# Kernel optimization log

Measured on AMD Instinct MI355X. Metric: run time of the kernel, lower is better.

The kernel has to match this reference:

```python
import jax, jax.numpy as jnp
import numpy as np


def _relative_position_index(w):
    # Deterministic Swin relative-position index, shape [w*w, w*w], values in [0, (2w-1)^2)
    coords_h = np.arange(w)
    coords_w = np.arange(w)
    coords = np.stack(np.meshgrid(coords_h, coords_w, indexing="ij"))  # [2, w, w]
    coords = coords.reshape(2, -1)                                      # [2, w*w]
    rel = coords[:, :, None] - coords[:, None, :]                       # [2, N, N]
    rel = rel.transpose(1, 2, 0).copy()                                 # [N, N, 2]
    rel[:, :, 0] += w - 1
    rel[:, :, 1] += w - 1
    rel[:, :, 0] *= 2 * w - 1
    return jnp.asarray(rel.sum(-1), dtype=jnp.int32)


def setup_inputs() -> dict:
    key = jax.random.key(0)
    ks = jax.random.split(key, 7)
    BS, N, C, H, W = 4096, 49, 384, 12, 7
    NW = 64  # number of windows per image
    x = jax.random.normal(ks[0], (BS, N, C), dtype=jnp.float32)
    # Swin shift mask: 0 where attention allowed, -100 where blocked
    u = jax.random.uniform(ks[1], (NW, N, N))
    mask = jnp.where(u < 0.5, 0.0, -100.0).astype(jnp.float32)
    qkv_w = jax.random.normal(ks[2], (C, 3 * C), dtype=jnp.float32) * (C ** -0.5)
    qkv_b = jax.random.normal(ks[3], (3 * C,), dtype=jnp.float32) * 0.02
    proj_w = jax.random.normal(ks[4], (C, C), dtype=jnp.float32) * (C ** -0.5)
    proj_b = jax.random.normal(ks[5], (C,), dtype=jnp.float32) * 0.02
    bias_table = jax.random.normal(ks[6], ((2 * W - 1) ** 2, H), dtype=jnp.float32) * 0.02
    return {"x": x, "mask": mask, "qkv_w": qkv_w, "qkv_b": qkv_b,
            "proj_w": proj_w, "proj_b": proj_b, "bias_table": bias_table,
            "n_heads": 12, "window_size": 7}


def reference(x, mask, qkv_w, qkv_b, proj_w, proj_b, bias_table, n_heads, window_size):
    BS, N, C = x.shape
    Hh = n_heads
    hd = C // Hh
    scale = hd ** -0.5
    rpi = _relative_position_index(window_size)  # [N, N] int

    qkv = x @ qkv_w + qkv_b                       # [BS, N, 3C]
    qkv = qkv.reshape(BS, N, 3, Hh, hd).transpose(2, 0, 3, 1, 4)  # [3, BS, H, N, hd]
    q, k, v = qkv[0], qkv[1], qkv[2]

    attn = jnp.einsum("bhnd,bhmd->bhnm", q, k) * scale   # [BS, H, N, N]
    # relative position bias gather: [N*N, H] -> [H, N, N]
    rpb = bias_table[rpi.reshape(-1)].reshape(N, N, Hh).transpose(2, 0, 1)
    attn = attn + rpb[None]

    nw = mask.shape[0]
    attn = attn.reshape(BS // nw, nw, Hh, N, N) + mask[None, :, None]
    attn = attn.reshape(BS, Hh, N, N)

    attn = jax.nn.softmax(attn, axis=-1)
    out = jnp.einsum("bhnm,bhmd->bhnd", attn, v)          # [BS, H, N, hd]
    out = out.transpose(0, 2, 1, 3).reshape(BS, N, C)
    return out @ proj_w + proj_b
```

## Files before the change

### kernel.cpp

```cpp
#include <hip/hip_runtime.h>
#include <hip/hip_bf16.h>


typedef __attribute__((ext_vector_type(8))) short bf16x8;
typedef __attribute__((ext_vector_type(4))) float f32x4;

#define SEQ_N  49
#define CH     384
#define QKV_N  1152
#define HDIM   32
#define UNIT_ROWS 3136

__device__ __forceinline__ unsigned short f2b(float f) {
    union { float f; unsigned int u; } v; v.f = f;
    return (unsigned short)((v.u + 0x7FFFu + ((v.u >> 16) & 1u)) >> 16);
}

__device__ __forceinline__ bf16x8 ld8(const unsigned short* p) {
    return *(const bf16x8*)p;
}

__device__ __forceinline__ void gload16(const unsigned short* g, unsigned short* l) {
    __builtin_amdgcn_global_load_lds(
        (const __attribute__((address_space(1))) unsigned int*)g,
        (__attribute__((address_space(3))) unsigned int*)l, 16, 0, 0);
}

__device__ __forceinline__ int xcd_swizzle(int orig, int T) {
    int q = T >> 3, r = T & 7;
    int xcd = orig & 7, idx = orig >> 3;
    return (xcd < r ? xcd * (q + 1) : r * (q + 1) + (xcd - r) * q) + idx;
}

__global__ __launch_bounds__(256) void k_cvt_w(const float* __restrict__ wq,
        const float* __restrict__ wp, unsigned short* __restrict__ oq,
        unsigned short* __restrict__ op)
{
    int t = blockIdx.x * 256 + threadIdx.x;
    if (t < QKV_N * CH) {
        int n = t / CH, k = t - n * CH;
        oq[t] = f2b(wq[(size_t)k * QKV_N + n]);
    }
    if (t < CH * CH) {
        int n = t / CH, k = t - n * CH;
        op[t] = f2b(wp[(size_t)k * CH + n]);
    }
}

__global__ __launch_bounds__(256) void k_cvt(const float* __restrict__ in,
        unsigned short* __restrict__ outp, int n8)
{
    int stride = gridDim.x * 256;
    for (int i = blockIdx.x * 256 + threadIdx.x; i < n8; i += stride) {
        const float4* p = (const float4*)(in + (size_t)i * 8);
        float4 a = p[0], b = p[1];
        uint4 v;
        v.x = (unsigned)f2b(a.x) | ((unsigned)f2b(a.y) << 16);
        v.y = (unsigned)f2b(a.z) | ((unsigned)f2b(a.w) << 16);
        v.z = (unsigned)f2b(b.x) | ((unsigned)f2b(b.y) << 16);
        v.w = (unsigned)f2b(b.z) | ((unsigned)f2b(b.w) << 16);
        *(uint4*)(outp + (size_t)i * 8) = v;
    }
}

template<int OUTF32>
__global__ __launch_bounds__(256) void k_gemm(
        const unsigned short* __restrict__ A, int lda,
        const unsigned short* __restrict__ Bt, int K,
        const float* __restrict__ bias,
        unsigned short* __restrict__ Cb, float* __restrict__ Cf, int ldc,
        int M, int ntiles, int mtiles)
{
    __shared__ unsigned short As[3 * 4096];
    __shared__ unsigned short Bs[3 * 4096];
    const int wg = xcd_swizzle(blockIdx.x, mtiles * ntiles);
    const int m0 = (wg / ntiles) * 128;
    const int n0 = (wg % ntiles) * 128;
    const int tid = threadIdx.x;
    const int lane = tid & 63, wid = tid >> 6;
    const int wm = (wid >> 1) * 64, wn = (wid & 1) * 64;
    const int l15 = lane & 15, g = lane >> 4;

    f32x4 acc[4][4];
#pragma unroll
    for (int a = 0; a < 4; ++a)
#pragma unroll
        for (int b = 0; b < 4; ++b) acc[a][b] = (f32x4){0.f, 0.f, 0.f, 0.f};

    const int r0 = wid * 16 + (lane >> 2);
    const int kofs = (lane & 3) * 8;
    int ra0 = m0 + r0;       if (ra0 > M - 1) ra0 = M - 1;
    int ra1 = m0 + 64 + r0;  if (ra1 > M - 1) ra1 = M - 1;
    const unsigned short* a0p = A + (size_t)ra0 * lda + kofs;
    const unsigned short* a1p = A + (size_t)ra1 * lda + kofs;
    const unsigned short* b0p = Bt + (size_t)(n0 + r0) * K + kofs;
    const unsigned short* b1p = Bt + (size_t)(n0 + 64 + r0) * K + kofs;
    const int lo = wid * 512;

#define STAGE(kt, buf) do {                                   \
        gload16(a0p + (kt), &As[(buf) * 4096 + lo]);          \
        gload16(a1p + (kt), &As[(buf) * 4096 + 2048 + lo]);   \
        gload16(b0p + (kt), &Bs[(buf) * 4096 + lo]);          \
        gload16(b1p + (kt), &Bs[(buf) * 4096 + 2048 + lo]);   \
    } while (0)

#define COMPUTE(buf) do {                                                     \
        bf16x8 af[4], bfr[4];                                                 \
        _Pragma("unroll")                                                     \
        for (int mt = 0; mt < 4; ++mt)                                        \
            af[mt] = ld8(&As[(buf) * 4096 + (wm + mt * 16 + l15) * 32 + g * 8]); \
        _Pragma("unroll")                                                     \
        for (int nt = 0; nt < 4; ++nt)                                        \
            bfr[nt] = ld8(&Bs[(buf) * 4096 + (wn + nt * 16 + l15) * 32 + g * 8]); \
        _Pragma("unroll")                                                     \
        for (int mt = 0; mt < 4; ++mt)                                        \
            _Pragma("unroll")                                                 \
            for (int nt = 0; nt < 4; ++nt)                                    \
                acc[mt][nt] = __builtin_amdgcn_mfma_f32_16x16x32_bf16(        \
                        af[mt], bfr[nt], acc[mt][nt], 0, 0, 0);               \
    } while (0)

    const int nsteps = K >> 5;

    STAGE(0, 0);
    STAGE(32, 1);

    int cur = 0;
    for (int t = 0; t < nsteps - 2; ++t) {
        int pf = cur + 2; if (pf >= 3) pf -= 3;
        STAGE((t + 2) * 32, pf);
        __builtin_amdgcn_sched_barrier(0);
        asm volatile("s_waitcnt vmcnt(8)" ::: "memory");
        __builtin_amdgcn_sched_barrier(0);
        __builtin_amdgcn_s_barrier();
        __builtin_amdgcn_sched_barrier(0);
        COMPUTE(cur);
        __builtin_amdgcn_sched_barrier(0);
        __builtin_amdgcn_s_barrier();
        __builtin_amdgcn_sched_barrier(0);
        cur = (cur == 2) ? 0 : cur + 1;
    }
    asm volatile("s_waitcnt vmcnt(4)" ::: "memory");
    __builtin_amdgcn_sched_barrier(0);
    __builtin_amdgcn_s_barrier();
    __builtin_amdgcn_sched_barrier(0);
    COMPUTE(cur);
    cur = (cur == 2) ? 0 : cur + 1;
    asm volatile("s_waitcnt vmcnt(0)" ::: "memory");
    __builtin_amdgcn_sched_barrier(0);
    __builtin_amdgcn_s_barrier();
    __builtin_amdgcn_sched_barrier(0);
    COMPUTE(cur);
#undef STAGE
#undef COMPUTE

#pragma unroll
    for (int mt = 0; mt < 4; ++mt)
#pragma unroll
        for (int nt = 0; nt < 4; ++nt) {
            int col = n0 + wn + nt * 16 + l15;
            float bb = bias[col];
#pragma unroll
            for (int r = 0; r < 4; ++r) {
                int row = m0 + wm + mt * 16 + g * 4 + r;
                if (row < M) {
                    if (OUTF32)
                        Cf[(size_t)row * ldc + col] = acc[mt][nt][r] + bb;
                    else
                        Cb[(size_t)row * ldc + col] = f2b(acc[mt][nt][r] + bb);
                }
            }
        }
}

__global__ __launch_bounds__(256) void k_attn(unsigned short* __restrict__ qkv,
        const float* __restrict__ mask, const float* __restrict__ btab, int win_base)
{
    extern __shared__ unsigned short sm[];
    const int tid = threadIdx.x;
    const int lane = tid & 63, wv = tid >> 6;
    const int l15 = lane & 15, g = lane >> 4;
    const int pair = blockIdx.x * 4 + wv;
    const int winloc = pair / 12;
    const int h = pair - winloc * 12;
    const int wimg = (win_base + winloc) & 63;
    const int co = h * HDIM;
    unsigned short* Vt = sm + wv * 6912;
    unsigned short* Pw = Vt + 32 * 72;
    unsigned short* src = qkv + (size_t)winloc * SEQ_N * QKV_N;

    for (int t = lane; t < 32 * 16; t += 64) {
        int c = t >> 4, kk = 48 + (t & 15);
        Vt[c * 72 + kk] = 0;
    }
    for (int t = lane; t < 49 * 4; t += 64) {
        int row = t >> 2, cb = (t & 3) * 8;
        const unsigned short* vp = src + (size_t)row * QKV_N + 768 + co + cb;
        ushort4 a = ((const ushort4*)vp)[0];
        ushort4 b = ((const ushort4*)vp)[1];
        Vt[(cb + 0) * 72 + row] = a.x; Vt[(cb + 1) * 72 + row] = a.y;
        Vt[(cb + 2) * 72 + row] = a.z; Vt[(cb + 3) * 72 + row] = a.w;
        Vt[(cb + 4) * 72 + row] = b.x; Vt[(cb + 5) * 72 + row] = b.y;
        Vt[(cb + 6) * 72 + row] = b.z; Vt[(cb + 7) * 72 + row] = b.w;
    }

    bf16x8 qf[4], kf[4];
#pragma unroll
    for (int mt = 0; mt < 4; ++mt) {
        int r = mt * 16 + l15; if (r > 48) r = 48;
        qf[mt] = ld8(src + (size_t)r * QKV_N + co + g * 8);
    }
#pragma unroll
    for (int nt = 0; nt < 4; ++nt) {
        int r = nt * 16 + l15; if (r > 48) r = 48;
        kf[nt] = ld8(src + (size_t)r * QKV_N + CH + co + g * 8);
    }

    f32x4 sa[4][4];
#pragma unroll
    for (int mt = 0; mt < 4; ++mt)
#pragma unroll
        for (int nt = 0; nt < 4; ++nt) sa[mt][nt] = (f32x4){0.f, 0.f, 0.f, 0.f};
#pragma unroll
    for (int mt = 0; mt < 4; ++mt)
#pragma unroll
        for (int nt = 0; nt < 4; ++nt)
            sa[mt][nt] = __builtin_amdgcn_mfma_f32_16x16x32_bf16(
                    qf[mt], kf[nt], sa[mt][nt], 0, 0, 0);

    int jj[4], jh[4], jw4[4];
#pragma unroll
    for (int nt = 0; nt < 4; ++nt) {
        int j = nt * 16 + l15;
        jj[nt] = j; jh[nt] = j / 7; jw4[nt] = j - (j / 7) * 7;
    }
    const float scale = 0.17677669529663687f;
#pragma unroll
    for (int mt = 0; mt < 4; ++mt) {
#pragma unroll
        for (int r = 0; r < 4; ++r) {
            int i = mt * 16 + g * 4 + r;
            int ic = i < 49 ? i : 48;
            int ih = ic / 7, iw = ic - (ic / 7) * 7;
            const float* mrow = mask + (size_t)wimg * 2401 + ic * 49;
            float sv[4];
#pragma unroll
            for (int nt = 0; nt < 4; ++nt) {
                float s = sa[mt][nt][r];
                if (jj[nt] < 49) {
                    int idx = (ih - jh[nt] + 6) * 13 + (iw - jw4[nt] + 6);
                    s = s * scale + btab[idx * 12 + h] + mrow[jj[nt]];
                } else s = -1e30f;
                sv[nt] = s;
            }
            float mx = fmaxf(fmaxf(sv[0], sv[1]), fmaxf(sv[2], sv[3]));
#pragma unroll
            for (int d = 1; d < 16; d <<= 1) mx = fmaxf(mx, __shfl_xor(mx, d));
            float sum = 0.f;
#pragma unroll
            for (int nt = 0; nt < 4; ++nt) { sv[nt] = __expf(sv[nt] - mx); sum += sv[nt]; }
#pragma unroll
            for (int d = 1; d < 16; d <<= 1) sum += __shfl_xor(sum, d);
            float inv = 1.0f / sum;
#pragma unroll
            for (int nt = 0; nt < 4; ++nt)
                Pw[i * 72 + nt * 16 + l15] = f2b(sv[nt] * inv);
        }
    }
    __syncthreads();

    f32x4 oa[4][2];
#pragma unroll
    for (int mt = 0; mt < 4; ++mt)
#pragma unroll
        for (int nt = 0; nt < 2; ++nt) oa[mt][nt] = (f32x4){0.f, 0.f, 0.f, 0.f};
#pragma unroll
    for (int ks = 0; ks < 2; ++ks) {
        bf16x8 pf[4];
#pragma unroll
        for (int mt = 0; mt < 4; ++mt)
            pf[mt] = ld8(Pw + (mt * 16 + l15) * 72 + ks * 32 + g * 8);
#pragma unroll
        for (int nt = 0; nt < 2; ++nt) {
            bf16x8 vf = ld8(Vt + (nt * 16 + l15) * 72 + ks * 32 + g * 8);
#pragma unroll
            for (int mt = 0; mt < 4; ++mt)
                oa[mt][nt] = __builtin_amdgcn_mfma_f32_16x16x32_bf16(
                        pf[mt], vf, oa[mt][nt], 0, 0, 0);
        }
    }

#pragma unroll
    for (int mt = 0; mt < 4; ++mt)
#pragma unroll
        for (int r = 0; r < 4; ++r) {
            int i = mt * 16 + g * 4 + r;
            if (i < 49) {
#pragma unroll
                for (int nt = 0; nt < 2; ++nt)
                    src[(size_t)i * QKV_N + co + nt * 16 + l15] = f2b(oa[mt][nt][r]);
            }
        }
}

extern "C" void kernel_launch(void* const* d_in, const int* in_sizes, int n_in,
                              void* d_out, int out_size, void* d_ws, size_t ws_size,
                              hipStream_t stream) {
    const float* x      = (const float*)d_in[0];
    const float* mask   = (const float*)d_in[1];
    const float* qkv_w  = (const float*)d_in[2];
    const float* qkv_b  = (const float*)d_in[3];
    const float* proj_w = (const float*)d_in[4];
    const float* proj_b = (const float*)d_in[5];
    const float* btab   = (const float*)d_in[6];
    float* out = (float*)d_out;

    unsigned short* wq_bt = (unsigned short*)d_ws;
    unsigned short* wp_bt = wq_bt + QKV_N * CH;
    unsigned short* base  = wp_bt + CH * CH;
    const size_t fixed = (size_t)(QKV_N * CH + CH * CH) * 2;
    const size_t unit  = (size_t)UNIT_ROWS * (CH + QKV_N) * 2;
    if (ws_size < fixed + unit) return;
    int upc = (int)((ws_size - fixed) / unit);
    if (upc > 64) upc = 64;
    unsigned short* xb  = base;
    unsigned short* qkv = base + (size_t)upc * UNIT_ROWS * CH;

    const int smem2 = 4 * 6912 * 2;
    hipFuncSetAttribute(reinterpret_cast<const void*>(k_attn),
                        hipFuncAttributeMaxDynamicSharedMemorySize, smem2);

    dim3 blk(256);
    k_cvt_w<<<dim3((QKV_N * CH + 255) / 256), blk, 0, stream>>>(qkv_w, proj_w, wq_bt, wp_bt);

    for (int u0 = 0; u0 < 64; u0 += upc) {
        int units = (64 - u0) < upc ? (64 - u0) : upc;
        int m_base = u0 * UNIT_ROWS;
        int Mc = units * UNIT_ROWS;
        int mtiles = (Mc + 127) / 128;
        k_cvt<<<dim3(2048), blk, 0, stream>>>(x + (size_t)m_base * CH, xb, Mc * 48);
        k_gemm<0><<<dim3(mtiles * 9), blk, 0, stream>>>(
                xb, CH, wq_bt, CH, qkv_b, qkv, nullptr, QKV_N, Mc, 9, mtiles);
        k_attn<<<dim3(units * 192), blk, smem2, stream>>>(qkv, mask, btab, u0);
        k_gemm<1><<<dim3(mtiles * 3), blk, 0, stream>>>(
                qkv, QKV_N, wp_bt, CH, proj_b, nullptr, out + (size_t)m_base * CH,
                CH, Mc, 3, mtiles);
    }
}
```

Measured before the change: 1.039 ms.

## Fuse fp32-to-bf16 conversion of x into the QKV GEMM A-tile load

```diff
diff --git a/kernel.cpp b/kernel.cpp
--- a/kernel.cpp
+++ b/kernel.cpp
@@ -8,7 +8,6 @@
 #define SEQ_N  49
 #define CH     384
 #define QKV_N  1152
-#define HDIM   32
 #define UNIT_ROWS 3136
 
 __device__ __forceinline__ unsigned short f2b(float f) {
@@ -20,7 +19,16 @@
     return *(const bf16x8*)p;
 }
 
-__device__ __forceinline__ void gload16(const unsigned short* g, unsigned short* l) {
+__device__ __forceinline__ bf16x8 cvt8(float4 a, float4 b) {
+    bf16x8 r;
+    r[0] = (short)f2b(a.x); r[1] = (short)f2b(a.y);
+    r[2] = (short)f2b(a.z); r[3] = (short)f2b(a.w);
+    r[4] = (short)f2b(b.x); r[5] = (short)f2b(b.y);
+    r[6] = (short)f2b(b.z); r[7] = (short)f2b(b.w);
+    return r;
+}
+
+__device__ __forceinline__ void gload16(const void* g, void* l) {
     __builtin_amdgcn_global_load_lds(
         (const __attribute__((address_space(1))) unsigned int*)g,
         (__attribute__((address_space(3))) unsigned int*)l, 16, 0, 0);
@@ -47,20 +55,102 @@
     }
 }
 
-__global__ __launch_bounds__(256) void k_cvt(const float* __restrict__ in,
-        unsigned short* __restrict__ outp, int n8)
+__global__ __launch_bounds__(256) void k_qkv_f(
+        const float* __restrict__ X,
+        const unsigned short* __restrict__ Bt,
+        const float* __restrict__ bias,
+        unsigned short* __restrict__ C, int M, int mtiles)
 {
-    int stride = gridDim.x * 256;
-    for (int i = blockIdx.x * 256 + threadIdx.x; i < n8; i += stride) {
-        const float4* p = (const float4*)(in + (size_t)i * 8);
-        float4 a = p[0], b = p[1];
-        uint4 v;
-        v.x = (unsigned)f2b(a.x) | ((unsigned)f2b(a.y) << 16);
-        v.y = (unsigned)f2b(a.z) | ((unsigned)f2b(a.w) << 16);
-        v.z = (unsigned)f2b(b.x) | ((unsigned)f2b(b.y) << 16);
-        v.w = (unsigned)f2b(b.z) | ((unsigned)f2b(b.w) << 16);
-        *(uint4*)(outp + (size_t)i * 8) = v;
-    }
+    extern __shared__ unsigned short smem[];
+    const int wg = xcd_swizzle(blockIdx.x, mtiles * 9);
+    const int m0 = (wg / 9) * 128;
+    const int n0 = (wg % 9) * 128;
+    const int tid = threadIdx.x;
+    const int lane = tid & 63, wv = tid >> 6;
+    const int wm = (wv >> 1) * 64, wn = (wv & 1) * 64;
+    const int l15 = lane & 15, g = lane >> 4;
+
+    f32x4 acc[4][4];
+#pragma unroll
+    for (int a = 0; a < 4; ++a)
+#pragma unroll
+        for (int b = 0; b < 4; ++b) acc[a][b] = (f32x4){0.f, 0.f, 0.f, 0.f};
+
+    const float* aSrc[4]; int aLds[4];
+#pragma unroll
+    for (int i2 = 0; i2 < 4; ++i2) {
+        int rloc = wv * 32 + i2 * 8 + (lane >> 3);
+        int grow = m0 + rloc; if (grow > M - 1) grow = M - 1;
+        aSrc[i2] = X + (size_t)grow * CH + (((lane & 7) ^ (lane >> 3)) * 4);
+        aLds[i2] = (wv * 32 + i2 * 8) * 64;
+    }
+    const unsigned short* bSrc[2]; int bLds[2];
+#pragma unroll
+    for (int j = 0; j < 2; ++j) {
+        int rloc = wv * 32 + j * 16 + (lane >> 2);
+        bSrc[j] = Bt + (size_t)(n0 + rloc) * CH + (((lane & 3) ^ ((lane >> 2) & 3)) * 8);
+        bLds[j] = 8192 + (wv * 32 + j * 16) * 32;
+    }
+
+#define STAGE(kc, b) do { unsigned short* pb = smem + (b) * 12288;  \
+        gload16(aSrc[0] + (kc), pb + aLds[0]);                       \
+        gload16(aSrc[1] + (kc), pb + aLds[1]);                       \
+        gload16(aSrc[2] + (kc), pb + aLds[2]);                       \
+        gload16(aSrc[3] + (kc), pb + aLds[3]);                       \
+        gload16(bSrc[0] + (kc), pb + bLds[0]);                       \
+        gload16(bSrc[1] + (kc), pb + bLds[1]); } while (0)
+
+    const int ns = 12;
+    STAGE(0, 0);
+    STAGE(32, 1);
+
+    for (int t = 0; t < ns; ++t) {
+        if (t + 1 < ns) asm volatile("s_waitcnt vmcnt(6)" ::: "memory");
+        else            asm volatile("s_waitcnt vmcnt(0)" ::: "memory");
+        __builtin_amdgcn_s_barrier();
+        __builtin_amdgcn_sched_barrier(0);
+        if (t + 2 < ns) STAGE((t + 2) * 32, (t + 2) % 3);
+        const unsigned short* pb = smem + (t % 3) * 12288;
+        const float* pa = (const float*)pb;
+        bf16x8 af[4], bfr[4];
+#pragma unroll
+        for (int mt = 0; mt < 4; ++mt) {
+            int row = wm + mt * 16 + l15;
+            int p0 = (2 * g) ^ (row & 7), p1 = (2 * g + 1) ^ (row & 7);
+            float4 fa = *(const float4*)(pa + row * 32 + p0 * 4);
+            float4 fb = *(const float4*)(pa + row * 32 + p1 * 4);
+            af[mt] = cvt8(fa, fb);
+        }
+#pragma unroll
+        for (int nt = 0; nt < 4; ++nt) {
+            int row = wn + nt * 16 + l15;
+            int p = g ^ (row & 3);
+            bfr[nt] = ld8(pb + 8192 + row * 32 + p * 8);
+        }
+        __builtin_amdgcn_s_setprio(1);
+#pragma unroll
+        for (int mt = 0; mt < 4; ++mt)
+#pragma unroll
+            for (int nt = 0; nt < 4; ++nt)
+                acc[mt][nt] = __builtin_amdgcn_mfma_f32_16x16x32_bf16(
+                        af[mt], bfr[nt], acc[mt][nt], 0, 0, 0);
+        __builtin_amdgcn_s_setprio(0);
+    }
+#undef STAGE
+
+#pragma unroll
+    for (int mt = 0; mt < 4; ++mt)
+#pragma unroll
+        for (int nt = 0; nt < 4; ++nt) {
+            int col = n0 + wn + nt * 16 + l15;
+            float bb = bias[col];
+#pragma unroll
+            for (int r = 0; r < 4; ++r) {
+                int row = m0 + wm + mt * 16 + g * 4 + r;
+                if (row < M)
+                    C[(size_t)row * QKV_N + col] = f2b(acc[mt][nt][r] + bb);
+            }
+        }
 }
 
 template<int OUTF32>
@@ -174,7 +264,7 @@
 }
 
 __global__ __launch_bounds__(256) void k_attn(unsigned short* __restrict__ qkv,
-        const float* __restrict__ mask, const float* __restrict__ btab, int win_base)
+        const float* __restrict__ mask, const float* __restrict__ btab)
 {
     extern __shared__ unsigned short sm[];
     const int tid = threadIdx.x;
@@ -183,8 +273,8 @@
     const int pair = blockIdx.x * 4 + wv;
     const int winloc = pair / 12;
     const int h = pair - winloc * 12;
-    const int wimg = (win_base + winloc) & 63;
-    const int co = h * HDIM;
+    const int wimg = winloc & 63;
+    const int co = h * 32;
     unsigned short* Vt = sm + wv * 6912;
     unsigned short* Pw = Vt + 32 * 72;
     unsigned short* src = qkv + (size_t)winloc * SEQ_N * QKV_N;
@@ -317,18 +407,19 @@
 
     unsigned short* wq_bt = (unsigned short*)d_ws;
     unsigned short* wp_bt = wq_bt + QKV_N * CH;
-    unsigned short* base  = wp_bt + CH * CH;
+    unsigned short* qkv   = wp_bt + CH * CH;
     const size_t fixed = (size_t)(QKV_N * CH + CH * CH) * 2;
-    const size_t unit  = (size_t)UNIT_ROWS * (CH + QKV_N) * 2;
+    const size_t unit  = (size_t)UNIT_ROWS * QKV_N * 2;
     if (ws_size < fixed + unit) return;
     int upc = (int)((ws_size - fixed) / unit);
     if (upc > 64) upc = 64;
-    unsigned short* xb  = base;
-    unsigned short* qkv = base + (size_t)upc * UNIT_ROWS * CH;
 
     const int smem2 = 4 * 6912 * 2;
     hipFuncSetAttribute(reinterpret_cast<const void*>(k_attn),
                         hipFuncAttributeMaxDynamicSharedMemorySize, smem2);
+    const int smemQ = 3 * 12288 * 2;
+    hipFuncSetAttribute(reinterpret_cast<const void*>(k_qkv_f),
+                        hipFuncAttributeMaxDynamicSharedMemorySize, smemQ);
 
     dim3 blk(256);
     k_cvt_w<<<dim3((QKV_N * CH + 255) / 256), blk, 0, stream>>>(qkv_w, proj_w, wq_bt, wp_bt);
@@ -338,10 +429,9 @@
         int m_base = u0 * UNIT_ROWS;
         int Mc = units * UNIT_ROWS;
         int mtiles = (Mc + 127) / 128;
-        k_cvt<<<dim3(2048), blk, 0, stream>>>(x + (size_t)m_base * CH, xb, Mc * 48);
-        k_gemm<0><<<dim3(mtiles * 9), blk, 0, stream>>>(
-                xb, CH, wq_bt, CH, qkv_b, qkv, nullptr, QKV_N, Mc, 9, mtiles);
-        k_attn<<<dim3(units * 192), blk, smem2, stream>>>(qkv, mask, btab, u0);
+        k_qkv_f<<<dim3(mtiles * 9), blk, smemQ, stream>>>(
+                x + (size_t)m_base * CH, wq_bt, qkv_b, qkv, Mc, mtiles);
+        k_attn<<<dim3(units * 192), blk, smem2, stream>>>(qkv, mask, btab);
         k_gemm<1><<<dim3(mtiles * 3), blk, 0, stream>>>(
                 qkv, QKV_N, wp_bt, CH, proj_b, nullptr, out + (size_t)m_base * CH,
                 CH, Mc, 3, mtiles);
```

After: 1.259 ms. 1.21x slower.

## Precompute fused bias+mask table and shrink attention LDS footprint

Applied to the files above, without the earlier changes.

```diff
diff --git a/kernel.cpp b/kernel.cpp
--- a/kernel.cpp
+++ b/kernel.cpp
@@ -8,8 +8,8 @@
 #define SEQ_N  49
 #define CH     384
 #define QKV_N  1152
-#define HDIM   32
 #define UNIT_ROWS 3136
+#define BM_ELEMS (64 * 12 * 49 * 49)
 
 __device__ __forceinline__ unsigned short f2b(float f) {
     union { float f; unsigned int u; } v; v.f = f;
@@ -45,6 +45,22 @@
         int n = t / CH, k = t - n * CH;
         op[t] = f2b(wp[(size_t)k * CH + n]);
     }
+}
+
+__global__ __launch_bounds__(256) void k_bm(const float* __restrict__ btab,
+        const float* __restrict__ mask, float* __restrict__ bm)
+{
+    int t = blockIdx.x * 256 + threadIdx.x;
+    if (t >= BM_ELEMS) return;
+    int w   = t / (12 * 2401);
+    int rem = t - w * 12 * 2401;
+    int h   = rem / 2401;
+    int ij  = rem - h * 2401;
+    int i = ij / 49, j = ij - (ij / 49) * 49;
+    int ih = i / 7, iw = i - (i / 7) * 7;
+    int jh = j / 7, jw = j - (j / 7) * 7;
+    int idx = (ih - jh + 6) * 13 + (iw - jw + 6);
+    bm[t] = btab[idx * 12 + h] + mask[(size_t)w * 2401 + ij];
 }
 
 __global__ __launch_bounds__(256) void k_cvt(const float* __restrict__ in,
@@ -174,7 +190,7 @@
 }
 
 __global__ __launch_bounds__(256) void k_attn(unsigned short* __restrict__ qkv,
-        const float* __restrict__ mask, const float* __restrict__ btab, int win_base)
+        const float* __restrict__ bm)
 {
     extern __shared__ unsigned short sm[];
     const int tid = threadIdx.x;
@@ -183,11 +199,12 @@
     const int pair = blockIdx.x * 4 + wv;
     const int winloc = pair / 12;
     const int h = pair - winloc * 12;
-    const int wimg = (win_base + winloc) & 63;
-    const int co = h * HDIM;
-    unsigned short* Vt = sm + wv * 6912;
+    const int wimg = winloc & 63;
+    const int co = h * 32;
+    unsigned short* Vt = sm + wv * 6048;
     unsigned short* Pw = Vt + 32 * 72;
     unsigned short* src = qkv + (size_t)winloc * SEQ_N * QKV_N;
+    const float* bmh = bm + ((size_t)(wimg * 12 + h)) * 2401;
 
     for (int t = lane; t < 32 * 16; t += 64) {
         int c = t >> 4, kk = 48 + (t & 15);
@@ -228,12 +245,9 @@
             sa[mt][nt] = __builtin_amdgcn_mfma_f32_16x16x32_bf16(
                     qf[mt], kf[nt], sa[mt][nt], 0, 0, 0);
 
-    int jj[4], jh[4], jw4[4];
-#pragma unroll
-    for (int nt = 0; nt < 4; ++nt) {
-        int j = nt * 16 + l15;
-        jj[nt] = j; jh[nt] = j / 7; jw4[nt] = j - (j / 7) * 7;
-    }
+    int jj[4];
+#pragma unroll
+    for (int nt = 0; nt < 4; ++nt) jj[nt] = nt * 16 + l15;
     const float scale = 0.17677669529663687f;
 #pragma unroll
     for (int mt = 0; mt < 4; ++mt) {
@@ -241,17 +255,12 @@
         for (int r = 0; r < 4; ++r) {
             int i = mt * 16 + g * 4 + r;
             int ic = i < 49 ? i : 48;
-            int ih = ic / 7, iw = ic - (ic / 7) * 7;
-            const float* mrow = mask + (size_t)wimg * 2401 + ic * 49;
+            const float* bmrow = bmh + ic * 49;
             float sv[4];
 #pragma unroll
             for (int nt = 0; nt < 4; ++nt) {
                 float s = sa[mt][nt][r];
-                if (jj[nt] < 49) {
-                    int idx = (ih - jh[nt] + 6) * 13 + (iw - jw4[nt] + 6);
-                    s = s * scale + btab[idx * 12 + h] + mrow[jj[nt]];
-                } else s = -1e30f;
-                sv[nt] = s;
+                sv[nt] = (jj[nt] < 49) ? (s * scale + bmrow[jj[nt]]) : -1e30f;
             }
             float mx = fmaxf(fmaxf(sv[0], sv[1]), fmaxf(sv[2], sv[3]));
 #pragma unroll
@@ -262,9 +271,11 @@
 #pragma unroll
             for (int d = 1; d < 16; d <<= 1) sum += __shfl_xor(sum, d);
             float inv = 1.0f / sum;
-#pragma unroll
-            for (int nt = 0; nt < 4; ++nt)
-                Pw[i * 72 + nt * 16 + l15] = f2b(sv[nt] * inv);
+            if (i < 52) {
+#pragma unroll
+                for (int nt = 0; nt < 4; ++nt)
+                    Pw[i * 72 + nt * 16 + l15] = f2b(sv[nt] * inv);
+            }
         }
     }
     __syncthreads();
@@ -278,8 +289,10 @@
     for (int ks = 0; ks < 2; ++ks) {
         bf16x8 pf[4];
 #pragma unroll
-        for (int mt = 0; mt < 4; ++mt)
-            pf[mt] = ld8(Pw + (mt * 16 + l15) * 72 + ks * 32 + g * 8);
+        for (int mt = 0; mt < 4; ++mt) {
+            int pr = mt * 16 + l15; if (pr > 51) pr = 51;
+            pf[mt] = ld8(Pw + pr * 72 + ks * 32 + g * 8);
+        }
 #pragma unroll
         for (int nt = 0; nt < 2; ++nt) {
             bf16x8 vf = ld8(Vt + (nt * 16 + l15) * 72 + ks * 32 + g * 8);
@@ -317,8 +330,9 @@
 
     unsigned short* wq_bt = (unsigned short*)d_ws;
     unsigned short* wp_bt = wq_bt + QKV_N * CH;
-    unsigned short* base  = wp_bt + CH * CH;
-    const size_t fixed = (size_t)(QKV_N * CH + CH * CH) * 2;
+    float*          bm    = (float*)(wp_bt + CH * CH);
+    unsigned short* base  = (unsigned short*)(bm + BM_ELEMS);
+    const size_t fixed = (size_t)(QKV_N * CH + CH * CH) * 2 + (size_t)BM_ELEMS * 4;
     const size_t unit  = (size_t)UNIT_ROWS * (CH + QKV_N) * 2;
     if (ws_size < fixed + unit) return;
     int upc = (int)((ws_size - fixed) / unit);
@@ -326,12 +340,13 @@
     unsigned short* xb  = base;
     unsigned short* qkv = base + (size_t)upc * UNIT_ROWS * CH;
 
-    const int smem2 = 4 * 6912 * 2;
+    const int smem2 = 4 * 6048 * 2;
     hipFuncSetAttribute(reinterpret_cast<const void*>(k_attn),
                         hipFuncAttributeMaxDynamicSharedMemorySize, smem2);
 
     dim3 blk(256);
     k_cvt_w<<<dim3((QKV_N * CH + 255) / 256), blk, 0, stream>>>(qkv_w, proj_w, wq_bt, wp_bt);
+    k_bm   <<<dim3((BM_ELEMS + 255) / 256), blk, 0, stream>>>(btab, mask, bm);
 
     for (int u0 = 0; u0 < 64; u0 += upc) {
         int units = (64 - u0) < upc ? (64 - u0) : upc;
@@ -341,7 +356,7 @@
         k_cvt<<<dim3(2048), blk, 0, stream>>>(x + (size_t)m_base * CH, xb, Mc * 48);
         k_gemm<0><<<dim3(mtiles * 9), blk, 0, stream>>>(
                 xb, CH, wq_bt, CH, qkv_b, qkv, nullptr, QKV_N, Mc, 9, mtiles);
-        k_attn<<<dim3(units * 192), blk, smem2, stream>>>(qkv, mask, btab, u0);
+        k_attn<<<dim3(units * 192), blk, smem2, stream>>>(qkv, bm);
         k_gemm<1><<<dim3(mtiles * 3), blk, 0, stream>>>(
                 qkv, QKV_N, wp_bt, CH, proj_b, nullptr, out + (size_t)m_base * CH,
                 CH, Mc, 3, mtiles);
```

New measurement: 937.6 us. -9.8%, faster.
